# Optimization experiments

Measured on AMD Instinct MI355X. Metric: run time of the kernel, lower is better.

Reference implementation:

```python
import jax, jax.numpy as jnp
import numpy as np

B, G, D, H, L, FFN = 4, 2048, 256, 8, 4, 1024
HD = D // H
BASE = 100.0
MASK_ID = -10.0
LN_EPS = 1e-5


def setup_inputs() -> dict:
    key = jax.random.key(0)
    ks = jax.random.split(key, 18)
    s = 0.02
    f32 = jnp.float32
    return {
        "x": jax.random.uniform(ks[0], (B, G), f32, 0.0, 8.0),
        "gene_emb": jax.random.normal(ks[1], (G, D), f32) * s,
        "Wq": jax.random.normal(ks[2], (L, D, D), f32) * s,
        "bq": jnp.zeros((L, D), f32),
        "Wk": jax.random.normal(ks[3], (L, D, D), f32) * s,
        "bk": jnp.zeros((L, D), f32),
        "Wv": jax.random.normal(ks[4], (L, D, D), f32) * s,
        "bv": jnp.zeros((L, D), f32),
        "ln1_g": jnp.ones((L, D), f32),
        "ln1_b": jnp.zeros((L, D), f32),
        "ln2_g": jnp.ones((L, D), f32),
        "ln2_b": jnp.zeros((L, D), f32),
        "WU": jax.random.normal(ks[5], (L, D, FFN), f32) * s,
        "bU": jnp.zeros((L, FFN), f32),
        "WV": jax.random.normal(ks[6], (L, FFN, D), f32) * s,
        "bV": jnp.zeros((L, D), f32),
        "Wo": jax.random.normal(ks[7], (D, 1), f32) * s,
        "bo": jnp.zeros((1,), f32),
    }


def _ln(x, g, b):
    mu = jnp.mean(x, axis=-1, keepdims=True)
    var = jnp.mean(jnp.square(x - mu), axis=-1, keepdims=True)
    return (x - mu) * jax.lax.rsqrt(var + LN_EPS) * g + b


def _linear_attn(z, Wq, bq, Wk, bk, Wv, bv):
    # feature_type='sqr': phi(u) = u**2; causal (compute_type='iter') linear attention
    q = jnp.square(z @ Wq + bq).reshape(B, G, H, HD)
    k = jnp.square(z @ Wk + bk).reshape(B, G, H, HD)
    v = (z @ Wv + bv).reshape(B, G, H, HD)
    kv = jnp.cumsum(jnp.einsum('bshm,bshd->bshmd', k, v), axis=1)  # prefix sums of k (x) v
    ksum = jnp.cumsum(k, axis=1)
    num = jnp.einsum('bshm,bshmd->bshd', q, kv)
    den = jnp.einsum('bshm,bshm->bsh', q, ksum)
    return (num / (den[..., None] + 1e-16)).reshape(B, G, D)


def reference(x, gene_emb, Wq, bq, Wk, bk, Wv, bv, ln1_g, ln1_b, ln2_g, ln2_b,
              WU, bU, WV, bV, Wo, bo):
    # rotary expression embedding
    inv_freq = 1.0 / BASE ** (jnp.arange(0, D, 2, dtype=jnp.float32) / D)  # [D/2]
    freqs = x[:, :, None] * inv_freq                                       # [B,G,D/2]
    ree = jnp.concatenate([jnp.sin(freqs), jnp.cos(freqs)], axis=-1)       # [B,G,D]
    ree = jnp.where((x == MASK_ID)[..., None], 0.0, ree)
    h = gene_emb[None] + ree
    for l in range(L):
        # pre-LN attention block
        h = h + _linear_attn(_ln(h, ln1_g[l], ln1_b[l]), Wq[l], bq[l], Wk[l], bk[l], Wv[l], bv[l])
        # pre-LN FFN block (exact erf gelu, as torch F.gelu default)
        z = _ln(h, ln2_g[l], ln2_b[l])
        h = h + jax.nn.gelu(z @ WU[l] + bU[l], approximate=False) @ WV[l] + bV[l]
    return (h @ Wo + bo)[..., 0]  # [B,G]
```

## Files before the change

kernel.cpp:

```cpp
#include <hip/hip_runtime.h>
#include <math.h>

constexpr int kB = 4, kG = 2048, kD = 256, kH = 8, kHD = 32, kL = 4, kFFN = 1024;
constexpr int kBG = kB * kG;
constexpr int kCHUNK = 64;
constexpr int kNC = kG / kCHUNK;
constexpr int kSUMSZ = kHD * kHD + kHD;
constexpr int kQKVN = 3 * kD;

typedef __bf16 bf16x8 __attribute__((ext_vector_type(8)));
typedef unsigned short ushort8 __attribute__((ext_vector_type(8)));
typedef float floatx4 __attribute__((ext_vector_type(4)));

__device__ __forceinline__ unsigned short f2bf(float f) {
  unsigned int u = __float_as_uint(f);
  u += 0x7fff + ((u >> 16) & 1);
  return (unsigned short)(u >> 16);
}
__device__ __forceinline__ float bf2f(unsigned short u) {
  return __uint_as_float(((unsigned int)u) << 16);
}

__device__ __forceinline__ void load_lds_16(const void* g, void* l) {
  __builtin_amdgcn_global_load_lds((const __attribute__((address_space(1))) void*)g,
                                   (__attribute__((address_space(3))) void*)l,
                                   16, 0, 0);
}

__global__ void embed_kernel(const float* __restrict__ x,
                             const float* __restrict__ ge,
                             float* __restrict__ h) {
  int idx = blockIdx.x * 256 + threadIdx.x;
  int d = idx & (kD - 1);
  int g = (idx >> 8) & (kG - 1);
  int b = idx >> 19;
  float xv = x[b * kG + g];
  int i = d & 127;
  float inv = expf(-(float)i * (4.6051701859880914f / 128.0f));
  float f = xv * inv;
  float r = (d < 128) ? sinf(f) : cosf(f);
  if (xv == -10.0f) r = 0.0f;
  h[idx] = ge[g * kD + d] + r;
}

__global__ void convert_weights_kernel(
    const float* __restrict__ Wq, const float* __restrict__ Wk,
    const float* __restrict__ Wv, const float* __restrict__ WU,
    const float* __restrict__ WV, const float* __restrict__ bq,
    const float* __restrict__ bk, const float* __restrict__ bv,
    unsigned short* __restrict__ Wqkv_t, unsigned short* __restrict__ WU_t,
    unsigned short* __restrict__ WV_t, float* __restrict__ bias_qkv) {
  int blk = blockIdx.x;
  if (blk >= kL * 704) {
    int idx = (blk - kL * 704) * 256 + threadIdx.x;
    if (idx < kL * kQKVN) {
      int l = idx / kQKVN, n = idx % kQKVN;
      float v = (n < 256) ? bq[l * 256 + n]
              : (n < 512) ? bk[l * 256 + n - 256]
                          : bv[l * 256 + n - 512];
      bias_qkv[idx] = v;
    }
    return;
  }
  int l = blk / 704, id = blk % 704;
  const float* src;
  unsigned short* dst;
  int Ksrc, Nsrc, kt, nt;
  if (id < 192) {
    int m = id >> 6, tid = id & 63;
    src = (m == 0 ? Wq : m == 1 ? Wk : Wv) + (size_t)l * 256 * 256;
    dst = Wqkv_t + (size_t)l * kQKVN * 256 + (size_t)m * 256 * 256;
    Ksrc = 256; Nsrc = 256; kt = tid >> 3; nt = tid & 7;
  } else if (id < 448) {
    int tid = id - 192;
    src = WU + (size_t)l * 256 * 1024;
    dst = WU_t + (size_t)l * 1024 * 256;
    Ksrc = 256; Nsrc = 1024; kt = tid >> 5; nt = tid & 31;
  } else {
    int tid = id - 448;
    src = WV + (size_t)l * 1024 * 256;
    dst = WV_t + (size_t)l * 256 * 1024;
    Ksrc = 1024; Nsrc = 256; kt = tid >> 3; nt = tid & 7;
  }
  __shared__ float s[32][33];
  int tx = threadIdx.x & 31, ty = threadIdx.x >> 5;
#pragma unroll
  for (int r = 0; r < 4; r++)
    s[ty + r * 8][tx] = src[(size_t)(kt * 32 + ty + r * 8) * Nsrc + nt * 32 + tx];
  __syncthreads();
#pragma unroll
  for (int r = 0; r < 4; r++)
    dst[(size_t)(nt * 32 + ty + r * 8) * Ksrc + kt * 32 + tx] =
        f2bf(s[tx][ty + r * 8]);
}

__global__ __launch_bounds__(256) void ln_kernel(
    const float* __restrict__ h, const float* __restrict__ gamma,
    const float* __restrict__ beta, unsigned short* __restrict__ z) {
  int w = threadIdx.x >> 6, lane = threadIdx.x & 63;
  size_t row = (size_t)blockIdx.x * 4 + w;
  float4 v = *(const float4*)&h[row * kD + lane * 4];
  float s = v.x + v.y + v.z + v.w;
  float sq = v.x * v.x + v.y * v.y + v.z * v.z + v.w * v.w;
#pragma unroll
  for (int o = 32; o > 0; o >>= 1) {
    s += __shfl_xor(s, o);
    sq += __shfl_xor(sq, o);
  }
  float mu = s * (1.0f / kD);
  float var = sq * (1.0f / kD) - mu * mu;
  float r = rsqrtf(var + 1e-5f);
  float4 g4 = *(const float4*)&gamma[lane * 4];
  float4 b4 = *(const float4*)&beta[lane * 4];
  float y0 = (v.x - mu) * r * g4.x + b4.x;
  float y1 = (v.y - mu) * r * g4.y + b4.y;
  float y2 = (v.z - mu) * r * g4.z + b4.z;
  float y3 = (v.w - mu) * r * g4.w + b4.w;
  unsigned int u0 = (unsigned int)f2bf(y0) | ((unsigned int)f2bf(y1) << 16);
  unsigned int u1 = (unsigned int)f2bf(y2) | ((unsigned int)f2bf(y3) << 16);
  uint2 uu; uu.x = u0; uu.y = u1;
  *(uint2*)&z[row * kD + lane * 4] = uu;
}

template <int EPI>
__global__ __launch_bounds__(256) void mfma_gemm(
    const unsigned short* __restrict__ A, const unsigned short* __restrict__ Bt,
    const float* __restrict__ bias, void* __restrict__ Cout,
    void* __restrict__ Cout2, const float* __restrict__ Cres,
    int M, int N, int K) {
  __shared__ unsigned short As[2][64 * 32];
  __shared__ unsigned short Bs[2][64 * 32];
  const int t = threadIdx.x;
  const int w = t >> 6, lane = t & 63;
  const int bm = blockIdx.y * 64, bn = blockIdx.x * 64;
  const int wm = (w >> 1) * 32, wn = (w & 1) * 32;

  const int srow = lane >> 2;
  const int skof = (lane & 3) * 8;
  const unsigned short* ap = A + (size_t)(bm + w * 16 + srow) * K + skof;
  const unsigned short* bp = Bt + (size_t)(bn + w * 16 + srow) * K + skof;

  floatx4 acc[2][2];
#pragma unroll
  for (int i = 0; i < 2; i++)
#pragma unroll
    for (int j = 0; j < 2; j++) acc[i][j] = (floatx4){0.f, 0.f, 0.f, 0.f};

  const int lm = lane & 15, lq = lane >> 4;
  const int nsteps = K >> 5;

  load_lds_16(ap, &As[0][w * 512]);
  load_lds_16(bp, &Bs[0][w * 512]);
  __syncthreads();

  for (int s = 0; s < nsteps; s++) {
    const int cur = s & 1, nxt = cur ^ 1;
    if (s + 1 < nsteps) {
      load_lds_16(ap + (s + 1) * 32, &As[nxt][w * 512]);
      load_lds_16(bp + (s + 1) * 32, &Bs[nxt][w * 512]);
    }
    const unsigned short* afp = &As[cur][(wm + lm) * 32 + lq * 8];
    const unsigned short* bfp = &Bs[cur][(wn + lm) * 32 + lq * 8];
    bf16x8 af[2], bfr[2];
#pragma unroll
    for (int i = 0; i < 2; i++)
      af[i] = __builtin_bit_cast(bf16x8,
          *reinterpret_cast<const ushort8*>(afp + i * 16 * 32));
#pragma unroll
    for (int j = 0; j < 2; j++)
      bfr[j] = __builtin_bit_cast(bf16x8,
          *reinterpret_cast<const ushort8*>(bfp + j * 16 * 32));
#pragma unroll
    for (int i = 0; i < 2; i++)
#pragma unroll
      for (int j = 0; j < 2; j++)
        acc[i][j] = __builtin_amdgcn_mfma_f32_16x16x32_bf16(af[i], bfr[j],
                                                            acc[i][j], 0, 0, 0);
    __syncthreads();
  }

  const int r0 = bm + wm + lq * 4;
  const int c0 = bn + wn + lm;
#pragma unroll
  for (int j = 0; j < 2; j++) {
    int col = c0 + j * 16;
    float bv = bias[col];
#pragma unroll
    for (int i = 0; i < 2; i++) {
      int rowb = r0 + i * 16;
#pragma unroll
      for (int r = 0; r < 4; r++) {
        int row = rowb + r;
        float v = acc[i][j][r] + bv;
        if (EPI == 1) {
          if (col < 512) {
            ((unsigned short*)Cout)[(size_t)row * 512 + col] = f2bf(v * v);
          } else {
            ((float*)Cout2)[(size_t)row * 256 + col - 512] = v;
          }
        } else if (EPI == 2) {
          float g = 0.5f * v * (1.0f + erff(v * 0.70710678118654752f));
          ((unsigned short*)Cout)[(size_t)row * N + col] = f2bf(g);
        } else {
          size_t idx = (size_t)row * N + col;
          ((float*)Cout)[idx] = Cres[idx] + v;
        }
      }
    }
  }
}

__global__ __launch_bounds__(256) void attn_sums_kernel(
    const unsigned short* __restrict__ qkb, const float* __restrict__ vbuf,
    float* __restrict__ sums) {
  int blk = blockIdx.x;
  int c = blk & (kNC - 1);
  int hh = (blk >> 5) & (kH - 1);
  int b = blk >> 8;
  int g0 = c * kCHUNK;
  __shared__ float ks[kCHUNK][kHD];
  __shared__ float vs[kCHUNK][kHD];
  int t = threadIdx.x;
  {
    int i = t >> 2, j8 = (t & 3) * 8;
    ushort8 kv = *(const ushort8*)&qkb[(size_t)(b * kG + g0 + i) * 512 + 256 +
                                       hh * kHD + j8];
#pragma unroll
    for (int e = 0; e < 8; e++) ks[i][j8 + e] = bf2f(kv[e]);
  }
#pragma unroll
  for (int r = 0; r < 2; r++) {
    int e = t + r * 256;
    int i = e >> 3, j = (e & 7) * 4;
    *(float4*)&vs[i][j] =
        *(const float4*)&vbuf[(size_t)(b * kG + g0 + i) * kD + hh * kHD + j];
  }
  __syncthreads();
  int m = t >> 3, n0 = (t & 7) * 4;
  float a0 = 0, a1 = 0, a2 = 0, a3 = 0;
  for (int i = 0; i < kCHUNK; i++) {
    float km = ks[i][m];
    float4 v4 = *(const float4*)&vs[i][n0];
    a0 = fmaf(km, v4.x, a0); a1 = fmaf(km, v4.y, a1);
    a2 = fmaf(km, v4.z, a2); a3 = fmaf(km, v4.w, a3);
  }
  float* outp = sums + (size_t)blk * kSUMSZ;
  *(float4*)&outp[m * kHD + n0] = make_float4(a0, a1, a2, a3);
  if (t < kHD) {
    float s = 0;
    for (int i = 0; i < kCHUNK; i++) s += ks[i][t];
    outp[kHD * kHD + t] = s;
  }
}

__global__ void attn_scan_kernel(float* __restrict__ sums) {
  int bh = blockIdx.x / 5, part = blockIdx.x % 5;
  int e = part * 256 + threadIdx.x;
  if (e >= kSUMSZ) return;
  float* base = sums + (size_t)bh * kNC * kSUMSZ + e;
  float v[kNC];
#pragma unroll
  for (int c = 0; c < kNC; c++) v[c] = base[(size_t)c * kSUMSZ];
  float run = 0;
#pragma unroll
  for (int c = 0; c < kNC; c++) {
    float tv = v[c];
    base[(size_t)c * kSUMSZ] = run;
    run += tv;
  }
}

__global__ __launch_bounds__(256) void attn_out_kernel(
    const unsigned short* __restrict__ qkb, const float* __restrict__ vbuf,
    const float* __restrict__ sums, float* __restrict__ h) {
  int blk = blockIdx.x;
  int c = blk & (kNC - 1);
  int hh = (blk >> 5) & (kH - 1);
  int b = blk >> 8;
  int g0 = c * kCHUNK;
  __shared__ unsigned short qb[kCHUNK * 40];
  __shared__ unsigned short kb[kCHUNK * 40];
  __shared__ float vs[kCHUNK][36];
  __shared__ float Sf[kHD][kHD];
  __shared__ float ksum[kHD];
  __shared__ float dinv_s[kCHUNK];
  __shared__ float Amat[kCHUNK][68];
  int t = threadIdx.x;
  {
    int i = t >> 2, j8 = (t & 3) * 8;
    const unsigned short* qrow = qkb + (size_t)(b * kG + g0 + i) * 512 + hh * kHD;
    *(ushort8*)&qb[i * 40 + j8] = *(const ushort8*)&qrow[j8];
    *(ushort8*)&kb[i * 40 + j8] = *(const ushort8*)&qrow[256 + j8];
  }
#pragma unroll
  for (int r = 0; r < 2; r++) {
    int e = t + r * 256;
    int i = e >> 3, j = (e & 7) * 4;
    *(float4*)&vs[i][j] =
        *(const float4*)&vbuf[(size_t)(b * kG + g0 + i) * kD + hh * kHD + j];
  }
  const float* sp = sums + (size_t)blk * kSUMSZ;
  *(float4*)&((float*)Sf)[t * 4] = *(const float4*)&sp[t * 4];
  if (t < 8) *(float4*)&ksum[t * 4] = *(const float4*)&sp[kHD * kHD + t * 4];
  __syncthreads();

  {
    const int w = t >> 6, lane = t & 63;
    const int lm = lane & 15, lq = lane >> 4;
    bf16x8 afr = __builtin_bit_cast(bf16x8,
        *reinterpret_cast<const ushort8*>(&qb[(16 * w + lm) * 40 + lq * 8]));
    floatx4 pacc[4];
#pragma unroll
    for (int jt = 0; jt < 4; jt++) {
      bf16x8 bfr = __builtin_bit_cast(bf16x8,
          *reinterpret_cast<const ushort8*>(&kb[(16 * jt + lm) * 40 + lq * 8]));
      pacc[jt] = __builtin_amdgcn_mfma_f32_16x16x32_bf16(
          afr, bfr, (floatx4){0.f, 0.f, 0.f, 0.f}, 0, 0, 0);
    }
#pragma unroll
    for (int jt = 0; jt < 4; jt++)
#pragma unroll
      for (int r = 0; r < 4; r++)
        Amat[16 * w + lq * 4 + r][16 * jt + lm] = pacc[jt][r];
#pragma unroll
    for (int r = 0; r < 4; r++) {
      int row = 16 * w + lq * 4 + r;
      float ps = 0.f;
#pragma unroll
      for (int jt = 0; jt < 4; jt++) {
        int j = 16 * jt + lm;
        ps += (j <= row) ? pacc[jt][r] : 0.f;
      }
      ps += bf2f(qb[row * 40 + lm]) * ksum[lm];
      ps += bf2f(qb[row * 40 + lm + 16]) * ksum[lm + 16];
      ps += __shfl_xor(ps, 1);
      ps += __shfl_xor(ps, 2);
      ps += __shfl_xor(ps, 4);
      ps += __shfl_xor(ps, 8);
      if (lm == 0) dinv_s[row] = 1.0f / (ps + 1e-16f);
    }
  }
  __syncthreads();

  float* hbase = h + (size_t)(b * kG + g0) * kD + hh * kHD;
#pragma unroll
  for (int uu = 0; uu < 2; uu++) {
    int u = t + uu * 256;
    int i = u >> 3, n0 = (u & 7) * 4;
    float ax = 0, ay = 0, az = 0, aw = 0;
#pragma unroll
    for (int m = 0; m < kHD; m++) {
      float qm = bf2f(qb[i * 40 + m]);
      float4 s4 = *(const float4*)&Sf[m][n0];
      ax = fmaf(qm, s4.x, ax); ay = fmaf(qm, s4.y, ay);
      az = fmaf(qm, s4.z, az); aw = fmaf(qm, s4.w, aw);
    }
    for (int j = 0; j <= i; j++) {
      float w = Amat[i][j];
      float4 vv = *(const float4*)&vs[j][n0];
      ax = fmaf(w, vv.x, ax); ay = fmaf(w, vv.y, ay);
      az = fmaf(w, vv.z, az); aw = fmaf(w, vv.w, aw);
    }
    float dinv = dinv_s[i];
    float* hp = hbase + (size_t)i * kD + n0;
    float4 old = *(const float4*)hp;
    *(float4*)hp = make_float4(old.x + ax * dinv, old.y + ay * dinv,
                               old.z + az * dinv, old.w + aw * dinv);
  }
}

__global__ __launch_bounds__(256) void final_kernel(
    const float* __restrict__ h, const float* __restrict__ Wo,
    const float* __restrict__ bo, float* __restrict__ out) {
  int w = threadIdx.x >> 6, lane = threadIdx.x & 63;
  size_t row = (size_t)blockIdx.x * 4 + w;
  float4 hv = *(const float4*)&h[row * kD + lane * 4];
  float4 wv = *(const float4*)&Wo[lane * 4];
  float s = hv.x * wv.x + hv.y * wv.y + hv.z * wv.z + hv.w * wv.w;
#pragma unroll
  for (int o = 32; o > 0; o >>= 1) s += __shfl_xor(s, o);
  if (lane == 0) out[row] = s + bo[0];
}

extern "C" void kernel_launch(void* const* d_in, const int* in_sizes, int n_in,
                              void* d_out, int out_size, void* d_ws, size_t ws_size,
                              hipStream_t stream) {
  const float* x    = (const float*)d_in[0];
  const float* ge   = (const float*)d_in[1];
  const float* Wq   = (const float*)d_in[2];
  const float* bq   = (const float*)d_in[3];
  const float* Wk   = (const float*)d_in[4];
  const float* bk   = (const float*)d_in[5];
  const float* Wv   = (const float*)d_in[6];
  const float* bv   = (const float*)d_in[7];
  const float* ln1g = (const float*)d_in[8];
  const float* ln1b = (const float*)d_in[9];
  const float* ln2g = (const float*)d_in[10];
  const float* ln2b = (const float*)d_in[11];
  const float* WU   = (const float*)d_in[12];
  const float* bU   = (const float*)d_in[13];
  const float* WV   = (const float*)d_in[14];
  const float* bV   = (const float*)d_in[15];
  const float* Wo   = (const float*)d_in[16];
  const float* bo   = (const float*)d_in[17];
  float* out = (float*)d_out;

  float* ws = (float*)d_ws;
  float*          h       = ws;
  unsigned short* zb      = (unsigned short*)(ws + 2097152);
  unsigned short* qkb     = (unsigned short*)(ws + 3145728);
  float*          vbuf    = ws + 5242880;
  unsigned short* u       = (unsigned short*)(ws + 3145728);
  float*          sums    = ws + 9437184;
  unsigned short* Wqkv_t  = (unsigned short*)(ws + 10518528);
  unsigned short* WU_t    = (unsigned short*)(ws + 10911744);
  unsigned short* WV_t    = (unsigned short*)(ws + 11436032);
  float*          bias_qkv= ws + 11960320;

  dim3 blk256(256);
  convert_weights_kernel<<<kL * 704 + 12, blk256, 0, stream>>>(
      Wq, Wk, Wv, WU, WV, bq, bk, bv, Wqkv_t, WU_t, WV_t, bias_qkv);
  embed_kernel<<<kBG * kD / 256, blk256, 0, stream>>>(x, ge, h);
  for (int l = 0; l < kL; l++) {
    ln_kernel<<<kBG / 4, blk256, 0, stream>>>(h, ln1g + l * kD, ln1b + l * kD, zb);
    mfma_gemm<1><<<dim3(kQKVN / 64, kBG / 64), blk256, 0, stream>>>(
        zb, Wqkv_t + (size_t)l * kQKVN * kD, bias_qkv + l * kQKVN, qkb, vbuf,
        nullptr, kBG, kQKVN, kD);
    attn_sums_kernel<<<kB * kH * kNC, blk256, 0, stream>>>(qkb, vbuf, sums);
    attn_scan_kernel<<<kB * kH * 5, blk256, 0, stream>>>(sums);
    attn_out_kernel<<<kB * kH * kNC, blk256, 0, stream>>>(qkb, vbuf, sums, h);
    ln_kernel<<<kBG / 4, blk256, 0, stream>>>(h, ln2g + l * kD, ln2b + l * kD, zb);
    mfma_gemm<2><<<dim3(kFFN / 64, kBG / 64), blk256, 0, stream>>>(
        zb, WU_t + (size_t)l * kFFN * kD, bU + l * kFFN, u, nullptr, nullptr,
        kBG, kFFN, kD);
    mfma_gemm<3><<<dim3(kD / 64, kBG / 64), blk256, 0, stream>>>(
        u, WV_t + (size_t)l * kD * kFFN, bV + l * kD, h, nullptr, h,
        kBG, kD, kFFN);
  }
  final_kernel<<<kBG / 4, blk256, 0, stream>>>(h, Wo, bo, out);
}
```

Baseline: 405.1 us.

## Compute attention output with MFMA and process two K-slices per GEMM step

The attention output kernel now builds a combined bf16 operand [masked P | q] and a transposed [V | S] operand in LDS. It then computes both the intra-chunk term and the prefix-state term with 16x16x32 MFMA instructions, replacing the scalar FMA loops over Amat and Sf. Separately, the GEMM loads two 32-wide K slices per pipeline stage, which halves the number of barriers per tile. The costs are lower precision, since P, V and the prefix sums are rounded to bf16, plus extra LDS use and scattered scalar LDS writes when transposing V.

```diff
diff --git a/kernel.cpp b/kernel.cpp
--- a/kernel.cpp
+++ b/kernel.cpp
@@ -128,8 +128,8 @@
     const float* __restrict__ bias, void* __restrict__ Cout,
     void* __restrict__ Cout2, const float* __restrict__ Cres,
     int M, int N, int K) {
-  __shared__ unsigned short As[2][64 * 32];
-  __shared__ unsigned short Bs[2][64 * 32];
+  __shared__ unsigned short As[2][2][64 * 32];
+  __shared__ unsigned short Bs[2][2][64 * 32];
   const int t = threadIdx.x;
   const int w = t >> 6, lane = t & 63;
   const int bm = blockIdx.y * 64, bn = blockIdx.x * 64;
@@ -147,35 +147,43 @@
     for (int j = 0; j < 2; j++) acc[i][j] = (floatx4){0.f, 0.f, 0.f, 0.f};
 
   const int lm = lane & 15, lq = lane >> 4;
-  const int nsteps = K >> 5;
-
-  load_lds_16(ap, &As[0][w * 512]);
-  load_lds_16(bp, &Bs[0][w * 512]);
+  const int nsteps = K >> 6;
+
+  load_lds_16(ap, &As[0][0][w * 512]);
+  load_lds_16(ap + 32, &As[0][1][w * 512]);
+  load_lds_16(bp, &Bs[0][0][w * 512]);
+  load_lds_16(bp + 32, &Bs[0][1][w * 512]);
   __syncthreads();
 
   for (int s = 0; s < nsteps; s++) {
     const int cur = s & 1, nxt = cur ^ 1;
     if (s + 1 < nsteps) {
-      load_lds_16(ap + (s + 1) * 32, &As[nxt][w * 512]);
-      load_lds_16(bp + (s + 1) * 32, &Bs[nxt][w * 512]);
-    }
-    const unsigned short* afp = &As[cur][(wm + lm) * 32 + lq * 8];
-    const unsigned short* bfp = &Bs[cur][(wn + lm) * 32 + lq * 8];
-    bf16x8 af[2], bfr[2];
-#pragma unroll
-    for (int i = 0; i < 2; i++)
-      af[i] = __builtin_bit_cast(bf16x8,
-          *reinterpret_cast<const ushort8*>(afp + i * 16 * 32));
-#pragma unroll
-    for (int j = 0; j < 2; j++)
-      bfr[j] = __builtin_bit_cast(bf16x8,
-          *reinterpret_cast<const ushort8*>(bfp + j * 16 * 32));
-#pragma unroll
-    for (int i = 0; i < 2; i++)
+      const int k1 = (s + 1) * 64;
+      load_lds_16(ap + k1, &As[nxt][0][w * 512]);
+      load_lds_16(ap + k1 + 32, &As[nxt][1][w * 512]);
+      load_lds_16(bp + k1, &Bs[nxt][0][w * 512]);
+      load_lds_16(bp + k1 + 32, &Bs[nxt][1][w * 512]);
+    }
+#pragma unroll
+    for (int kc = 0; kc < 2; kc++) {
+      const unsigned short* afp = &As[cur][kc][(wm + lm) * 32 + lq * 8];
+      const unsigned short* bfp = &Bs[cur][kc][(wn + lm) * 32 + lq * 8];
+      bf16x8 af[2], bfr[2];
+#pragma unroll
+      for (int i = 0; i < 2; i++)
+        af[i] = __builtin_bit_cast(bf16x8,
+            *reinterpret_cast<const ushort8*>(afp + i * 16 * 32));
 #pragma unroll
       for (int j = 0; j < 2; j++)
-        acc[i][j] = __builtin_amdgcn_mfma_f32_16x16x32_bf16(af[i], bfr[j],
-                                                            acc[i][j], 0, 0, 0);
+        bfr[j] = __builtin_bit_cast(bf16x8,
+            *reinterpret_cast<const ushort8*>(bfp + j * 16 * 32));
+#pragma unroll
+      for (int i = 0; i < 2; i++)
+#pragma unroll
+        for (int j = 0; j < 2; j++)
+          acc[i][j] = __builtin_amdgcn_mfma_f32_16x16x32_bf16(af[i], bfr[j],
+                                                              acc[i][j], 0, 0, 0);
+    }
     __syncthreads();
   }
 
@@ -278,37 +286,43 @@
   int hh = (blk >> 5) & (kH - 1);
   int b = blk >> 8;
   int g0 = c * kCHUNK;
-  __shared__ unsigned short qb[kCHUNK * 40];
+  constexpr int PST = 104;
+  __shared__ unsigned short Pq[kCHUNK * PST];
   __shared__ unsigned short kb[kCHUNK * 40];
-  __shared__ float vs[kCHUNK][36];
-  __shared__ float Sf[kHD][kHD];
+  __shared__ unsigned short VtS[kHD * PST];
   __shared__ float ksum[kHD];
   __shared__ float dinv_s[kCHUNK];
-  __shared__ float Amat[kCHUNK][68];
   int t = threadIdx.x;
   {
     int i = t >> 2, j8 = (t & 3) * 8;
     const unsigned short* qrow = qkb + (size_t)(b * kG + g0 + i) * 512 + hh * kHD;
-    *(ushort8*)&qb[i * 40 + j8] = *(const ushort8*)&qrow[j8];
+    *(ushort8*)&Pq[i * PST + 64 + j8] = *(const ushort8*)&qrow[j8];
     *(ushort8*)&kb[i * 40 + j8] = *(const ushort8*)&qrow[256 + j8];
   }
 #pragma unroll
   for (int r = 0; r < 2; r++) {
     int e = t + r * 256;
-    int i = e >> 3, j = (e & 7) * 4;
-    *(float4*)&vs[i][j] =
-        *(const float4*)&vbuf[(size_t)(b * kG + g0 + i) * kD + hh * kHD + j];
+    int j = e >> 3, n0 = (e & 7) * 4;
+    float4 vv = *(const float4*)&vbuf[(size_t)(b * kG + g0 + j) * kD + hh * kHD + n0];
+    VtS[(n0 + 0) * PST + j] = f2bf(vv.x);
+    VtS[(n0 + 1) * PST + j] = f2bf(vv.y);
+    VtS[(n0 + 2) * PST + j] = f2bf(vv.z);
+    VtS[(n0 + 3) * PST + j] = f2bf(vv.w);
   }
   const float* sp = sums + (size_t)blk * kSUMSZ;
-  *(float4*)&((float*)Sf)[t * 4] = *(const float4*)&sp[t * 4];
-  if (t < 8) *(float4*)&ksum[t * 4] = *(const float4*)&sp[kHD * kHD + t * 4];
+#pragma unroll
+  for (int r = 0; r < 4; r++) {
+    int e = t + r * 256;
+    VtS[(e & 31) * PST + 64 + (e >> 5)] = f2bf(sp[e]);
+  }
+  if (t < kHD) ksum[t] = sp[kHD * kHD + t];
   __syncthreads();
 
+  const int w = t >> 6, lane = t & 63;
+  const int lm = lane & 15, lq = lane >> 4;
   {
-    const int w = t >> 6, lane = t & 63;
-    const int lm = lane & 15, lq = lane >> 4;
     bf16x8 afr = __builtin_bit_cast(bf16x8,
-        *reinterpret_cast<const ushort8*>(&qb[(16 * w + lm) * 40 + lq * 8]));
+        *reinterpret_cast<const ushort8*>(&Pq[(16 * w + lm) * PST + 64 + lq * 8]));
     floatx4 pacc[4];
 #pragma unroll
     for (int jt = 0; jt < 4; jt++) {
@@ -320,8 +334,10 @@
 #pragma unroll
     for (int jt = 0; jt < 4; jt++)
 #pragma unroll
-      for (int r = 0; r < 4; r++)
-        Amat[16 * w + lq * 4 + r][16 * jt + lm] = pacc[jt][r];
+      for (int r = 0; r < 4; r++) {
+        int row = 16 * w + lq * 4 + r, col = 16 * jt + lm;
+        Pq[row * PST + col] = (col <= row) ? f2bf(pacc[jt][r]) : 0;
+      }
 #pragma unroll
     for (int r = 0; r < 4; r++) {
       int row = 16 * w + lq * 4 + r;
@@ -331,8 +347,8 @@
         int j = 16 * jt + lm;
         ps += (j <= row) ? pacc[jt][r] : 0.f;
       }
-      ps += bf2f(qb[row * 40 + lm]) * ksum[lm];
-      ps += bf2f(qb[row * 40 + lm + 16]) * ksum[lm + 16];
+      ps += bf2f(Pq[row * PST + 64 + lm]) * ksum[lm];
+      ps += bf2f(Pq[row * PST + 80 + lm]) * ksum[lm + 16];
       ps += __shfl_xor(ps, 1);
       ps += __shfl_xor(ps, 2);
       ps += __shfl_xor(ps, 4);
@@ -342,30 +358,29 @@
   }
   __syncthreads();
 
-  float* hbase = h + (size_t)(b * kG + g0) * kD + hh * kHD;
-#pragma unroll
-  for (int uu = 0; uu < 2; uu++) {
-    int u = t + uu * 256;
-    int i = u >> 3, n0 = (u & 7) * 4;
-    float ax = 0, ay = 0, az = 0, aw = 0;
-#pragma unroll
-    for (int m = 0; m < kHD; m++) {
-      float qm = bf2f(qb[i * 40 + m]);
-      float4 s4 = *(const float4*)&Sf[m][n0];
-      ax = fmaf(qm, s4.x, ax); ay = fmaf(qm, s4.y, ay);
-      az = fmaf(qm, s4.z, az); aw = fmaf(qm, s4.w, aw);
-    }
-    for (int j = 0; j <= i; j++) {
-      float w = Amat[i][j];
-      float4 vv = *(const float4*)&vs[j][n0];
-      ax = fmaf(w, vv.x, ax); ay = fmaf(w, vv.y, ay);
-      az = fmaf(w, vv.z, az); aw = fmaf(w, vv.w, aw);
-    }
-    float dinv = dinv_s[i];
-    float* hp = hbase + (size_t)i * kD + n0;
-    float4 old = *(const float4*)hp;
-    *(float4*)hp = make_float4(old.x + ax * dinv, old.y + ay * dinv,
-                               old.z + az * dinv, old.w + aw * dinv);
+  {
+    floatx4 oacc[2];
+    oacc[0] = (floatx4){0.f, 0.f, 0.f, 0.f};
+    oacc[1] = (floatx4){0.f, 0.f, 0.f, 0.f};
+#pragma unroll
+    for (int kc = 0; kc < 3; kc++) {
+      bf16x8 af = __builtin_bit_cast(bf16x8,
+          *reinterpret_cast<const ushort8*>(&Pq[(16 * w + lm) * PST + kc * 32 + lq * 8]));
+#pragma unroll
+      for (int jt = 0; jt < 2; jt++) {
+        bf16x8 bfv = __builtin_bit_cast(bf16x8,
+            *reinterpret_cast<const ushort8*>(&VtS[(16 * jt + lm) * PST + kc * 32 + lq * 8]));
+        oacc[jt] = __builtin_amdgcn_mfma_f32_16x16x32_bf16(af, bfv, oacc[jt], 0, 0, 0);
+      }
+    }
+#pragma unroll
+    for (int jt = 0; jt < 2; jt++)
+#pragma unroll
+      for (int r = 0; r < 4; r++) {
+        int row = 16 * w + lq * 4 + r, col = 16 * jt + lm;
+        float* hp = h + (size_t)(b * kG + g0 + row) * kD + hh * kHD + col;
+        *hp += oacc[jt][r] * dinv_s[row];
+      }
   }
 }
 
```

New measurement: 366.0 us. 1.11x faster.
